# Performance work log

Hardware: AMD Instinct MI355X
Metric: run time of the kernel (lower is better)

## Reference

```python
import jax, jax.numpy as jnp
import numpy as np

BOX_LOWER, BOX_UPPER = -3.0, 3.0
EPS = 1e-7


def base_quartic_spline(t):
    # Piecewise quartic B-spline-like basis on |t| with breakpoints 0.5, 1.5, 2.5.
    ta = jnp.abs(t)
    # branch 0: |t| < 0.5
    z0 = ta + 0.5
    r0 = (11.0 + z0 * (12.0 + z0 * (-6.0 + z0 * (-12.0 + 6.0 * z0)))) / 24.0
    # branch 1: 0.5 <= |t| < 1.5
    z1 = 1.5 - ta
    r1 = (1.0 + z1 * (4.0 + z1 * (6.0 + z1 * (4.0 - 4.0 * z1)))) / 24.0
    # branch 2: 1.5 <= |t| < 2.5
    z2 = (2.5 - ta) * (2.5 - ta)
    r2 = z2 * z2 / 24.0
    out = jnp.where(ta >= 0.5, r1, r0)
    out = jnp.where(ta >= 1.5, r2, out)
    return jnp.where(ta >= 2.5, jnp.zeros_like(ta), out)


def setup_inputs() -> dict:
    key = jax.random.key(0)
    k1, k2 = jax.random.split(key)
    b, f, n, h, w = 16, 16, 64, 64, 64
    x = jax.random.normal(k1, (b, f, h, w), dtype=jnp.float32)
    weight_tensor = jax.random.uniform(k2, (f, n), dtype=jnp.float32)
    nodes = jnp.linspace(BOX_LOWER, BOX_UPPER, n, dtype=jnp.float32)
    return {"x": x, "weight_tensor": weight_tensor, "nodes": nodes}


def reference(x, weight_tensor, nodes):
    n = nodes.shape[0]
    scale = (BOX_UPPER - BOX_LOWER) / (n - 1)
    # (b, f, n, h, w) broadcasted scaled distance to nodes
    t = (x[:, :, None, :, :] - nodes.reshape(1, 1, n, 1, 1)) / scale
    basis = base_quartic_spline(t)
    y = jnp.einsum('bfnhw,fn->bfhw', basis, jnp.exp(weight_tensor))
    return jnp.sum(jnp.log(y + EPS))
```

## Files before the change

kernel.cpp:

```cpp
#include <hip/hip_runtime.h>

constexpr int F_ = 16, N_ = 64;
constexpr int TOTAL = 16 * 16 * 64 * 64;
constexpr int VEC = TOTAL / 4;
constexpr int THREADS = 1024;
constexpr int BLOCKS = VEC / THREADS;
constexpr float LOWER = -3.0f, UPPER = 3.0f;

__global__ __launch_bounds__(THREADS) void spline_partial(
    const float* __restrict__ x,
    const float* __restrict__ weight,
    float* __restrict__ partials)
{
    __shared__ float ew[F_ * N_];
    const int tid = threadIdx.x;
    ew[tid] = __expf(weight[tid]);
    __syncthreads();

    const int idx4 = blockIdx.x * THREADS + tid;
    const float4 v = reinterpret_cast<const float4*>(x)[idx4];
    const float* __restrict__ ewf = &ew[(blockIdx.x & (F_ - 1)) * N_];

    const float vals[4] = {v.x, v.y, v.z, v.w};
    float local = 0.0f;

    #pragma unroll
    for (int j = 0; j < 4; ++j) {
        const float u = fmaf(vals[j], 10.5f, 31.5f);
        const float r = rintf(u);
        const float s = u - r;
        const int n0 = (int)r - 2;

        const float p = 0.5f - s, q = 0.5f + s;
        const float p2 = p * p, q2 = q * q, s2 = s * s;
        float w[5];
        w[0] = p2 * p2;
        w[1] = 1.0f + p * (4.0f + p * (6.0f + p * (4.0f - 4.0f * p)));
        w[2] = fmaf(s2, fmaf(s2, 6.0f, -15.0f), 14.375f);
        w[3] = 1.0f + q * (4.0f + q * (6.0f + q * (4.0f - 4.0f * q)));
        w[4] = q2 * q2;

        float y = 0.0f;
        #pragma unroll
        for (int d = 0; d < 5; ++d) {
            const int n = n0 + d;
            const bool valid = ((unsigned)n < (unsigned)N_);
            const float wd = valid ? w[d] : 0.0f;
            y += wd * ewf[valid ? n : 0];
        }
        local += __logf(fmaf(y, 1.0f / 24.0f, 1e-7f));
    }

    #pragma unroll
    for (int off = 32; off > 0; off >>= 1)
        local += __shfl_down(local, off, 64);

    __shared__ float wpart[THREADS / 64];
    if ((tid & 63) == 0) wpart[tid >> 6] = local;
    __syncthreads();
    if (tid == 0) {
        float s = 0.0f;
        #pragma unroll
        for (int i = 0; i < THREADS / 64; ++i) s += wpart[i];
        partials[blockIdx.x] = s;
    }
}

__global__ __launch_bounds__(256) void reduce_partials(
    const float* __restrict__ partials, float* __restrict__ out)
{
    const int tid = threadIdx.x;
    float v = partials[tid];
    #pragma unroll
    for (int off = 32; off > 0; off >>= 1)
        v += __shfl_down(v, off, 64);
    __shared__ float wpart[4];
    if ((tid & 63) == 0) wpart[tid >> 6] = v;
    __syncthreads();
    if (tid == 0) out[0] = wpart[0] + wpart[1] + wpart[2] + wpart[3];
}

extern "C" void kernel_launch(void* const* d_in, const int* in_sizes, int n_in,
                              void* d_out, int out_size, void* d_ws, size_t ws_size,
                              hipStream_t stream) {
    const float* x      = (const float*)d_in[0];
    const float* weight = (const float*)d_in[1];
    float* out      = (float*)d_out;
    float* partials = (float*)d_ws;

    spline_partial<<<BLOCKS, THREADS, 0, stream>>>(x, weight, partials);
    reduce_partials<<<1, 256, 0, stream>>>(partials, out);
}
```

Measured before the change: 60.39 us.

## Replace shared-memory weight table with per-wave shuffles and drop block syncs

Each wave now loads its feature's 64 exp-weights into registers (one per lane) and fetches the five needed nodes with cross-lane shuffles, replacing the LDS table and its barrier. Blocks shrink to 256 threads, and each wave writes its own partial sum directly, which removes the second barrier and the per-block LDS reduction. The final reduction kernel grows to 1024 threads reading float4 to cover four times as many partials. Shuffles cost ds_bpermute-style instructions per lookup, and four times more partials must be written and reduced.

Result: no change. 61.24 us (+1.4%).

```diff
diff --git a/kernel.cpp b/kernel.cpp
--- a/kernel.cpp
+++ b/kernel.cpp
@@ -3,27 +3,26 @@
 constexpr int F_ = 16, N_ = 64;
 constexpr int TOTAL = 16 * 16 * 64 * 64;
 constexpr int VEC = TOTAL / 4;
-constexpr int THREADS = 1024;
+constexpr int THREADS = 256;
 constexpr int BLOCKS = VEC / THREADS;
-constexpr float LOWER = -3.0f, UPPER = 3.0f;
+constexpr int NPART = BLOCKS * (THREADS / 64);
 
 __global__ __launch_bounds__(THREADS) void spline_partial(
     const float* __restrict__ x,
     const float* __restrict__ weight,
     float* __restrict__ partials)
 {
-    __shared__ float ew[F_ * N_];
-    const int tid = threadIdx.x;
-    ew[tid] = __expf(weight[tid]);
-    __syncthreads();
+    const int tid  = threadIdx.x;
+    const int lane = tid & 63;
+
+    const int f = (blockIdx.x >> 2) & (F_ - 1);
+    const float roww = __expf(weight[f * N_ + lane]);
 
     const int idx4 = blockIdx.x * THREADS + tid;
     const float4 v = reinterpret_cast<const float4*>(x)[idx4];
-    const float* __restrict__ ewf = &ew[(blockIdx.x & (F_ - 1)) * N_];
+    const float vals[4] = {v.x, v.y, v.z, v.w};
 
-    const float vals[4] = {v.x, v.y, v.z, v.w};
     float local = 0.0f;
-
     #pragma unroll
     for (int j = 0; j < 4; ++j) {
         const float u = fmaf(vals[j], 10.5f, 31.5f);
@@ -44,9 +43,9 @@
         #pragma unroll
         for (int d = 0; d < 5; ++d) {
             const int n = n0 + d;
-            const bool valid = ((unsigned)n < (unsigned)N_);
-            const float wd = valid ? w[d] : 0.0f;
-            y += wd * ewf[valid ? n : 0];
+            const float ev = __shfl(roww, n & (N_ - 1), 64);
+            const float wd = ((unsigned)n < (unsigned)N_) ? w[d] : 0.0f;
+            y = fmaf(wd, ev, y);
         }
         local += __logf(fmaf(y, 1.0f / 24.0f, 1e-7f));
     }
@@ -54,30 +53,29 @@
     #pragma unroll
     for (int off = 32; off > 0; off >>= 1)
         local += __shfl_down(local, off, 64);
-
-    __shared__ float wpart[THREADS / 64];
-    if ((tid & 63) == 0) wpart[tid >> 6] = local;
-    __syncthreads();
-    if (tid == 0) {
-        float s = 0.0f;
-        #pragma unroll
-        for (int i = 0; i < THREADS / 64; ++i) s += wpart[i];
-        partials[blockIdx.x] = s;
-    }
+    if (lane == 0)
+        partials[(idx4 >> 6)] = local;
 }
 
-__global__ __launch_bounds__(256) void reduce_partials(
+__global__ __launch_bounds__(1024) void reduce_partials(
     const float* __restrict__ partials, float* __restrict__ out)
 {
     const int tid = threadIdx.x;
-    float v = partials[tid];
+    const float4 v = reinterpret_cast<const float4*>(partials)[tid];
+    float s = (v.x + v.y) + (v.z + v.w);
     #pragma unroll
     for (int off = 32; off > 0; off >>= 1)
-        v += __shfl_down(v, off, 64);
-    __shared__ float wpart[4];
-    if ((tid & 63) == 0) wpart[tid >> 6] = v;
+        s += __shfl_down(s, off, 64);
+
+    __shared__ float wpart[16];
+    if ((tid & 63) == 0) wpart[tid >> 6] = s;
     __syncthreads();
-    if (tid == 0) out[0] = wpart[0] + wpart[1] + wpart[2] + wpart[3];
+    if (tid == 0) {
+        float t = 0.0f;
+        #pragma unroll
+        for (int i = 0; i < 16; ++i) t += wpart[i];
+        out[0] = t;
+    }
 }
 
 extern "C" void kernel_launch(void* const* d_in, const int* in_sizes, int n_in,
@@ -89,5 +87,5 @@
     float* partials = (float*)d_ws;
 
     spline_partial<<<BLOCKS, THREADS, 0, stream>>>(x, weight, partials);
-    reduce_partials<<<1, 256, 0, stream>>>(partials, out);
+    reduce_partials<<<1, 1024, 0, stream>>>(partials, out);
 }
```
